# Optimization experiments

Measured on AMD Instinct MI355X. Metric: run time of the kernel, lower is better.

The kernel has to match this reference:

```python
import jax, jax.numpy as jnp
import numpy as np

NH = 12        # main attention heads (head_dim = 64)
SNH = 4        # scorer self-attention heads
ALPHA = 0.1    # static survival-score weight
EPS = 1e-8


def _linear(x, w, b):
    # torch nn.Linear: y = x @ W^T + b
    return x @ w.T + b


def _mha(x, in_w, in_b, out_w, out_b, n_heads, maskf):
    # torch nn.MultiheadAttention (batch_first, eval mode)
    B, S, D = x.shape
    hd = D // n_heads
    qkv = _linear(x, in_w, in_b)                      # [B,S,3D]
    q, k, v = jnp.split(qkv, 3, axis=-1)
    sp = lambda t: t.reshape(B, S, n_heads, hd).transpose(0, 2, 1, 3)
    q, k, v = sp(q), sp(k), sp(v)                     # [B,h,S,hd]
    scores = jnp.einsum('bhqd,bhkd->bhqk', q, k) / jnp.asarray(np.sqrt(hd), x.dtype)
    scores = jnp.where(maskf[:, None, None, :] > 0, scores, jnp.asarray(-1e9, x.dtype))
    aw = jax.nn.softmax(scores, axis=-1)
    o = jnp.einsum('bhqk,bhkd->bhqd', aw, v).transpose(0, 2, 1, 3).reshape(B, S, D)
    return _linear(o, out_w, out_b)


def _survival_scores(x, maskf, sp_w, sp_b, sa_in_w, sa_in_b, sa_out_w, sa_out_b,
                     nw1, nb1, nw2, nb2, mw1, mb1, mw2, mb2, dw1, db1, dw2, db2):
    h = _linear(x, sp_w, sp_b)                        # [B,S,256]
    h = _mha(h, sa_in_w, sa_in_b, sa_out_w, sa_out_b, SNH, maskf)
    n = jax.nn.softplus(_linear(jax.nn.relu(_linear(h, nw1, nb1)), nw2, nb2))[..., 0]
    mu = jax.nn.sigmoid(_linear(jax.nn.relu(_linear(h, mw1, mb1)), mw2, mb2))[..., 0]
    delta = jax.nn.relu(_linear(jax.nn.relu(_linear(h, dw1, db1)), dw2, db2))[..., 0]
    # S = log(N) + log(mu / mu_c) - delta, with mu_c = 1.0
    return jnp.log(n + EPS) + jnp.log(mu + EPS) - delta


def setup_inputs() -> dict:
    key = jax.random.key(0)
    ks = iter(jax.random.split(key, 40))
    W = lambda shape: jax.random.normal(next(ks), shape, jnp.float32) * 0.05
    Z = lambda shape: jnp.zeros(shape, jnp.float32)
    B, S, H, I = 2, 2048, 768, 256
    inp = {
        'x': jax.random.normal(next(ks), (B, S, H), jnp.float32),
        'mask': jnp.ones((B, S), jnp.int32),
        'qw': W((H, H)), 'qb': Z((H,)),
        'kw': W((H, H)), 'kb': Z((H,)),
        'vw': W((H, H)), 'vb': Z((H,)),
        'ow': W((H, H)), 'ob': Z((H,)),
        'sp_w': W((I, H)), 'sp_b': Z((I,)),
        'sa_in_w': W((3 * I, I)), 'sa_in_b': Z((3 * I,)),
        'sa_out_w': W((I, I)), 'sa_out_b': Z((I,)),
        'nw1': W((I // 2, I)), 'nb1': Z((I // 2,)), 'nw2': W((1, I // 2)), 'nb2': Z((1,)),
        'mw1': W((I // 2, I)), 'mb1': Z((I // 2,)), 'mw2': W((1, I // 2)), 'mb2': Z((1,)),
        'dw1': W((I // 2, I)), 'db1': Z((I // 2,)), 'dw2': W((1, I // 2)), 'db2': Z((1,)),
    }
    return inp


def reference(x, mask, qw, qb, kw, kb, vw, vb, ow, ob,
              sp_w, sp_b, sa_in_w, sa_in_b, sa_out_w, sa_out_b,
              nw1, nb1, nw2, nb2, mw1, mb1, mw2, mb2, dw1, db1, dw2, db2):
    B, S, H = x.shape
    hd = H // NH
    maskf = mask.astype(x.dtype)
    # Q/K/V projections -> [B,h,S,hd]
    sp = lambda t: t.reshape(B, S, NH, hd).transpose(0, 2, 1, 3)
    q = sp(_linear(x, qw, qb))
    k = sp(_linear(x, kw, kb))
    v = sp(_linear(x, vw, vb))
    scores = jnp.einsum('bhqd,bhkd->bhqk', q, k) / jnp.asarray(np.sqrt(hd), x.dtype)
    # survival-score bias (broadcast over heads and query positions)
    surv = _survival_scores(x, maskf, sp_w, sp_b, sa_in_w, sa_in_b, sa_out_w, sa_out_b,
                            nw1, nb1, nw2, nb2, mw1, mb1, mw2, mb2, dw1, db1, dw2, db2)
    scores = scores + ALPHA * surv[:, None, None, :]
    scores = scores + (1.0 - maskf)[:, None, None, :] * -1e9
    aw = jax.nn.softmax(scores, axis=-1)
    out = jnp.einsum('bhqk,bhkd->bhqd', aw, v).transpose(0, 2, 1, 3).reshape(B, S, H)
    return _linear(out, ow, ob)
```

## Files before the change

### kernel.cpp

```cpp
#include <hip/hip_runtime.h>
#include <math.h>

typedef __bf16 bf16;
typedef __bf16 bfrag __attribute__((ext_vector_type(8)));
typedef __bf16 bf4 __attribute__((ext_vector_type(4)));
typedef float f4 __attribute__((ext_vector_type(4)));
typedef float f16v __attribute__((ext_vector_type(16)));
typedef unsigned uint2v __attribute__((ext_vector_type(2)));

#define LOG2E 1.4426950408889634f

#define DEV static __device__ __forceinline__

DEV f4 MFMA(bfrag a, bfrag b, f4 c) {
  return __builtin_amdgcn_mfma_f32_16x16x32_bf16(a, b, c, 0, 0, 0);
}
DEV f16v MFMA32(bfrag a, bfrag b, f16v c) {
  return __builtin_amdgcn_mfma_f32_32x32x16_bf16(a, b, c, 0, 0, 0);
}
DEV float ex2(float x) { return __builtin_amdgcn_exp2f(x); }
DEV uint2v pl32(unsigned a, unsigned b) {
  return __builtin_amdgcn_permlane32_swap(a, b, false, false);
}
DEV void gload_lds16(const bf16* g, bf16* l) {
  __builtin_amdgcn_global_load_lds(
      (const __attribute__((address_space(1))) void*)g,
      (__attribute__((address_space(3))) void*)l, 16, 0, 0);
}
DEV void gload_lds4(const float* g, float* l) {
  __builtin_amdgcn_global_load_lds(
      (const __attribute__((address_space(1))) void*)g,
      (__attribute__((address_space(3))) void*)l, 4, 0, 0);
}

__global__ __launch_bounds__(256) void pack_all(
    const float* __restrict__ x, const float* __restrict__ qw, const float* __restrict__ kw,
    const float* __restrict__ vw, const float* __restrict__ ow, const float* __restrict__ sp_w,
    const float* __restrict__ sa_in_w, const float* __restrict__ sa_out_w,
    const float* __restrict__ nw1, const float* __restrict__ mw1, const float* __restrict__ dw1,
    const float* __restrict__ sp_b, const float* __restrict__ qb, const float* __restrict__ kb,
    const float* __restrict__ vb,
    const float* __restrict__ nb1, const float* __restrict__ mb1, const float* __restrict__ db1,
    const int* __restrict__ mask,
    bf16* __restrict__ xb, bf16* __restrict__ wfused, bf16* __restrict__ wob,
    bf16* __restrict__ sainb, bf16* __restrict__ saoutb,
    bf16* __restrict__ w1pack, float* __restrict__ bfused, float* __restrict__ b1pack,
    float* __restrict__ maskBias) {
  int bid = blockIdx.x;
  int tid = threadIdx.x;
  const float* src = nullptr;
  bf16* dst = nullptr;
  int rel = 0;
  if (bid < 3072)      { src = x;       dst = xb;                   rel = bid; }
  else if (bid < 3264) { src = sp_w;    dst = wfused;               rel = bid - 3072; }
  else if (bid < 3840) { src = qw;      dst = wfused + 196608;      rel = bid - 3264; }
  else if (bid < 4416) { src = kw;      dst = wfused + 786432;      rel = bid - 3840; }
  else if (bid < 4992) { src = vw;      dst = wfused + 1376256;     rel = bid - 4416; }
  else if (bid < 5568) { src = ow;      dst = wob;                  rel = bid - 4992; }
  else if (bid < 5760) { src = sa_in_w; dst = sainb;                rel = bid - 5568; }
  else if (bid < 5824) { src = sa_out_w;dst = saoutb;               rel = bid - 5760; }
  else if (bid < 5856) { src = nw1;     dst = w1pack;               rel = bid - 5824; }
  else if (bid < 5888) { src = mw1;     dst = w1pack + 32768;       rel = bid - 5856; }
  else if (bid < 5920) { src = dw1;     dst = w1pack + 2 * 32768;   rel = bid - 5888; }
  else if (bid == 5920) {
    for (int t = tid; t < 640; t += 256) {
      const float* s;
      int j;
      if (t < 64)       { s = sp_b; j = t; }
      else if (t < 256) { s = qb;   j = t - 64; }
      else if (t < 448) { s = kb;   j = t - 256; }
      else              { s = vb;   j = t - 448; }
      reinterpret_cast<float4*>(bfused)[t] = reinterpret_cast<const float4*>(s)[j];
    }
    return;
  } else if (bid == 5921) {
    if (tid < 96) {
      int which = tid / 32, j = tid % 32;
      const float* s = which == 0 ? nb1 : (which == 1 ? mb1 : db1);
      reinterpret_cast<float4*>(b1pack)[tid] = reinterpret_cast<const float4*>(s)[j];
    }
    return;
  } else {
    int idx = (bid - 5922) * 256 + tid;
    int4 m = reinterpret_cast<const int4*>(mask)[idx];
    float4 o;
    o.x = m.x > 0 ? 0.f : -1e9f * LOG2E;
    o.y = m.y > 0 ? 0.f : -1e9f * LOG2E;
    o.z = m.z > 0 ? 0.f : -1e9f * LOG2E;
    o.w = m.w > 0 ? 0.f : -1e9f * LOG2E;
    reinterpret_cast<float4*>(maskBias)[idx] = o;
    return;
  }
  int i = rel * 256 + tid;
  float4 v = reinterpret_cast<const float4*>(src)[i];
  bf4 o;
  o[0] = (bf16)v.x; o[1] = (bf16)v.y; o[2] = (bf16)v.z; o[3] = (bf16)v.w;
  reinterpret_cast<bf4*>(dst)[i] = o;
}

template<int OUTF32, int RELU>
__global__ __launch_bounds__(256) void gemm_nt(
    const bf16* __restrict__ A, int lda,
    const bf16* __restrict__ W, int ldw,
    const float* __restrict__ bias,
    void* __restrict__ C, int ldc,
    int N64, int K) {
  int lane = threadIdx.x & 63;
  int w = threadIdx.x >> 6;
  int lrow = lane & 15, lgrp = lane >> 4;
  int tn = blockIdx.x % N64, tm = blockIdx.x / N64;
  int m0 = tm * 64 + (w >> 1) * 32;
  int n0 = tn * 64 + (w & 1) * 32;
  const bf16* Ab = A + (size_t)m0 * lda + lgrp * 8;
  const bf16* Wb = W + (size_t)n0 * ldw + lgrp * 8;
  f4 acc[2][2] = {};
  for (int k0 = 0; k0 < K; k0 += 32) {
    bfrag a0 = *(const bfrag*)(Ab + (size_t)lrow * lda + k0);
    bfrag a1 = *(const bfrag*)(Ab + (size_t)(lrow + 16) * lda + k0);
    bfrag b0 = *(const bfrag*)(Wb + (size_t)lrow * ldw + k0);
    bfrag b1 = *(const bfrag*)(Wb + (size_t)(lrow + 16) * ldw + k0);
    acc[0][0] = MFMA(a0, b0, acc[0][0]);
    acc[0][1] = MFMA(a0, b1, acc[0][1]);
    acc[1][0] = MFMA(a1, b0, acc[1][0]);
    acc[1][1] = MFMA(a1, b1, acc[1][1]);
  }
#pragma unroll
  for (int mi = 0; mi < 2; mi++)
#pragma unroll
    for (int nj = 0; nj < 2; nj++) {
      int col = n0 + nj * 16 + lrow;
      float bv = bias[col];
      int rowb = m0 + mi * 16 + lgrp * 4;
#pragma unroll
      for (int i = 0; i < 4; i++) {
        float v = acc[mi][nj][i] + bv;
        if (RELU) v = fmaxf(v, 0.f);
        if (OUTF32)
          ((float*)C)[(size_t)(rowb + i) * ldc + col] = v;
        else
          ((bf16*)C)[(size_t)(rowb + i) * ldc + col] = (bf16)v;
      }
    }
}

template<int OUTF32>
__global__ __launch_bounds__(256, 2) void gemm_big(
    const bf16* __restrict__ A,
    const bf16* __restrict__ W,
    const float* __restrict__ bias,
    void* __restrict__ C, int ldc,
    int N128, int K) {
  __shared__ char smem[65536];
  int lane = threadIdx.x & 63;
  int w = threadIdx.x >> 6;
  int lrow = lane & 15, lgrp = lane >> 4;
  int tn = blockIdx.x % N128, tm = blockIdx.x / N128;
  int m0 = tm * 128, n0 = tn * 128;

  int srow = lane >> 3;
  int sslot = (lane & 7) ^ srow;

  auto stage = [&](int bufb, int k0) {
#pragma unroll
    for (int j = 0; j < 4; j++) {
      int rb = (w * 4 + j) * 8 + srow;
      gload_lds16(A + (size_t)(m0 + rb) * K + k0 + sslot * 8,
                  (bf16*)(smem + bufb + (w * 4 + j) * 1024));
      gload_lds16(W + (size_t)(n0 + rb) * K + k0 + sslot * 8,
                  (bf16*)(smem + bufb + 16384 + (w * 4 + j) * 1024));
    }
  };

  f4 acc[4][4] = {};
  int swz = (lrow & 7) << 4;
  int mbase = (w >> 1) * 64, nbase = (w & 1) * 64;

  stage(0, 0);
  __syncthreads();
  int buf = 0;
  int nt = K / 64;
  for (int t = 0; t < nt; t++) {
    int nbuf = buf ^ 32768;
    if (t + 1 < nt) stage(nbuf, (t + 1) * 64);
    const char* As = smem + buf;
    const char* Ws = smem + buf + 16384;
#pragma unroll
    for (int kb = 0; kb < 128; kb += 64) {
      bfrag a[4], b[4];
#pragma unroll
      for (int i = 0; i < 4; i++) {
        a[i] = *(const bfrag*)(As + (mbase + i * 16 + lrow) * 128 + ((kb + lgrp * 16) ^ swz));
        b[i] = *(const bfrag*)(Ws + (nbase + i * 16 + lrow) * 128 + ((kb + lgrp * 16) ^ swz));
      }
#pragma unroll
      for (int mi = 0; mi < 4; mi++)
#pragma unroll
        for (int nj = 0; nj < 4; nj++)
          acc[mi][nj] = MFMA(a[mi], b[nj], acc[mi][nj]);
    }
    __syncthreads();
    buf = nbuf;
  }

#pragma unroll
  for (int mi = 0; mi < 4; mi++)
#pragma unroll
    for (int nj = 0; nj < 4; nj++) {
      int col = n0 + nbase + nj * 16 + lrow;
      float bv = bias[col];
      int rowb = m0 + mbase + mi * 16 + lgrp * 4;
#pragma unroll
      for (int i = 0; i < 4; i++) {
        float v = acc[mi][nj][i] + bv;
        if (OUTF32)
          ((float*)C)[(size_t)(rowb + i) * ldc + col] = v;
        else
          ((bf16*)C)[(size_t)(rowb + i) * ldc + col] = (bf16)v;
      }
    }
}

__global__ __launch_bounds__(256) void vtrans(const bf16* __restrict__ V, int rs, int coff,
                                              bf16* __restrict__ Vt, int H, int S) {
  int nst = S / 64;
  int st = blockIdx.x % nst;
  int h = (blockIdx.x / nst) % H;
  int b = blockIdx.x / (nst * H);
  __shared__ bf16 tile[64][72];
  int t = threadIdx.x;
  int r = t >> 2, c = t & 3;
  const bf16* src = V + ((size_t)b * S + st * 64 + r) * rs + coff + h * 64 + c * 16;
  bfrag v0 = *(const bfrag*)(src);
  bfrag v1 = *(const bfrag*)(src + 8);
  *(bfrag*)&tile[r][c * 16] = v0;
  *(bfrag*)&tile[r][c * 16 + 8] = v1;
  __syncthreads();
  bf16* dst = Vt + (((size_t)b * H + h) * 64 + r) * S + st * 64 + c * 16;
  bfrag o0, o1;
#pragma unroll
  for (int j = 0; j < 8; j++) {
    o0[j] = tile[c * 16 + j][r];
    o1[j] = tile[c * 16 + 8 + j][r];
  }
  *(bfrag*)dst = o0;
  *(bfrag*)(dst + 8) = o1;
}

template<int SPLIT, int PARTIAL>
__global__ __launch_bounds__(256) void flash12_k(
    const bf16* __restrict__ Q, const bf16* __restrict__ Kp, int rs,
    const bf16* __restrict__ Vt, const float* __restrict__ bias,
    bf16* __restrict__ O, int ors,
    bf16* __restrict__ Opart, float* __restrict__ Lpart,
    int H, int S, float scale, int Bc) {
  int nqt = S / 128;
  int nwg8 = (gridDim.x >> 3);
  int bid0 = blockIdx.x;
  int bid = (bid0 & 7) * nwg8 + (bid0 >> 3);
  int qt = bid % nqt;
  int hh = (bid / nqt) % H;
  int b = (bid / (nqt * H)) % Bc;
  int sp = bid / (nqt * H * Bc);
  int lane = threadIdx.x & 63, w = threadIdx.x >> 6;
  int l31 = lane & 31, hf = lane >> 5;
  int q0 = qt * 128 + w * 32;
  const int kchunk = S / SPLIT;
  int k_beg = sp * kchunk;
  int swzl = (l31 & 7) << 4;

  const bf16* Qb = Q + ((size_t)b * S + q0 + l31) * rs + hh * 64 + hf * 8;
  bfrag qf[4];
#pragma unroll
  for (int c = 0; c < 4; c++) qf[c] = *(const bfrag*)(Qb + 16 * c);

  const bf16* gK0 = Kp + ((size_t)b * S + k_beg) * rs + hh * 64;
  const bf16* gV0 = Vt + (((size_t)b * H + hh) * 64) * (size_t)S + k_beg;
  const float* biasb = bias + (size_t)b * S + k_beg;

  __shared__ bf16 KT[3][4096];
  __shared__ bf16 VT[3][4096];
  __shared__ float BL[3][64];

  f16v acc0, acc1;
#pragma unroll
  for (int r = 0; r < 16; r++) { acc0[r] = 0.f; acc1[r] = 0.f; }
  float lrun = 0.f;

  int srow = lane >> 3;
  int sel = ((lane & 7) ^ srow) * 8;
  int r0 = (w * 2) * 8 + srow;
  int r1 = (w * 2 + 1) * 8 + srow;

  auto stage = [&](int bb, int trel) {
    const bf16* gK = gK0 + (size_t)trel * 64 * rs;
    const bf16* gV = gV0 + trel * 64;
    gload_lds16(gK + (size_t)r0 * rs + sel, KT[bb] + (w * 2) * 512);
    gload_lds16(gK + (size_t)r1 * rs + sel, KT[bb] + (w * 2 + 1) * 512);
    gload_lds16(gV + (size_t)r0 * S + sel, VT[bb] + (w * 2) * 512);
    gload_lds16(gV + (size_t)r1 * S + sel, VT[bb] + (w * 2 + 1) * 512);
    gload_lds4(biasb + trel * 64 + lane, BL[bb]);
  };

  const int nt = kchunk / 64;
  stage(0, 0);
  if (nt > 1) stage(1, 1);

  int buf = 0;
  for (int t = 0; t < nt; t++) {
    if (t + 1 < nt) asm volatile("s_waitcnt vmcnt(5)" ::: "memory");
    else            asm volatile("s_waitcnt vmcnt(0)" ::: "memory");
    __builtin_amdgcn_s_barrier();
    __builtin_amdgcn_sched_barrier(0);
    if (t + 2 < nt) stage(buf == 0 ? 2 : buf - 1, t + 2);

    const char* KTb = (const char*)KT[buf];
    const char* VTb = (const char*)VT[buf];
    const float* BLb = BL[buf];

    f4 blo[4], bhi[4];
#pragma unroll
    for (int g = 0; g < 4; g++) {
      blo[g] = *(const f4*)(BLb + g * 8 + hf * 4);
      bhi[g] = *(const f4*)(BLb + 32 + g * 8 + hf * 4);
    }

    f16v s_lo, s_hi;
#pragma unroll
    for (int r = 0; r < 16; r++) { s_lo[r] = 0.f; s_hi[r] = 0.f; }
    __builtin_amdgcn_s_setprio(1);
#pragma unroll
    for (int c = 0; c < 4; c++) {
      int colb = 32 * c + 16 * hf;
      bfrag klo = *(const bfrag*)(KTb + l31 * 128 + (colb ^ swzl));
      bfrag khi = *(const bfrag*)(KTb + (32 + l31) * 128 + (colb ^ swzl));
      s_lo = MFMA32(klo, qf[c], s_lo);
      s_hi = MFMA32(khi, qf[c], s_hi);
    }
    __builtin_amdgcn_s_setprio(0);

#pragma unroll
    for (int r = 0; r < 16; r++) {
      s_lo[r] = ex2(s_lo[r] * scale + blo[r >> 2][r & 3]);
      s_hi[r] = ex2(s_hi[r] * scale + bhi[r >> 2][r & 3]);
    }
    float rsum = s_lo[0] + s_hi[0];
#pragma unroll
    for (int r = 1; r < 16; r++) rsum += s_lo[r] + s_hi[r];
    rsum += __shfl_xor(rsum, 32);
    lrun += rsum;

    bfrag pb[4];
#pragma unroll
    for (int cc = 0; cc < 4; cc++) {
      const f16v& sv = (cc < 2) ? s_lo : s_hi;
      int rb = (cc & 1) * 8;
      unsigned lo0, lo1, hi0, hi1;
      asm("v_cvt_pk_bf16_f32 %0, %1, %2" : "=v"(lo0) : "v"(sv[rb + 0]), "v"(sv[rb + 1]));
      asm("v_cvt_pk_bf16_f32 %0, %1, %2" : "=v"(lo1) : "v"(sv[rb + 2]), "v"(sv[rb + 3]));
      asm("v_cvt_pk_bf16_f32 %0, %1, %2" : "=v"(hi0) : "v"(sv[rb + 4]), "v"(sv[rb + 5]));
      asm("v_cvt_pk_bf16_f32 %0, %1, %2" : "=v"(hi1) : "v"(sv[rb + 6]), "v"(sv[rb + 7]));
      uint2v e0 = pl32(lo0, hi0);
      uint2v e1 = pl32(lo1, hi1);
      union { bfrag v; unsigned u[4]; } pu;
      pu.u[0] = e0[0]; pu.u[1] = e1[0]; pu.u[2] = e0[1]; pu.u[3] = e1[1];
      pb[cc] = pu.v;
    }

    __builtin_amdgcn_s_setprio(1);
#pragma unroll
    for (int c = 0; c < 4; c++) {
      int colb = 32 * c + 16 * hf;
      bfrag v0 = *(const bfrag*)(VTb + l31 * 128 + (colb ^ swzl));
      bfrag v1 = *(const bfrag*)(VTb + (32 + l31) * 128 + (colb ^ swzl));
      acc0 = MFMA32(v0, pb[c], acc0);
      acc1 = MFMA32(v1, pb[c], acc1);
    }
    __builtin_amdgcn_s_setprio(0);

    buf = (buf == 2) ? 0 : buf + 1;
  }

  int q = q0 + l31;
  if (PARTIAL) {
    bf16* op = Opart + ((((size_t)sp * Bc + b) * H + hh) * S + q) * 64 + hf * 4;
#pragma unroll
    for (int g = 0; g < 4; g++) {
      bf4 v0, v1;
#pragma unroll
      for (int i = 0; i < 4; i++) {
        v0[i] = (bf16)acc0[4 * g + i];
        v1[i] = (bf16)acc1[4 * g + i];
      }
      *(bf4*)(op + g * 8) = v0;
      *(bf4*)(op + 32 + g * 8) = v1;
    }
    if (hf == 0)
      Lpart[(((size_t)sp * Bc + b) * H + hh) * S + q] = lrun;
  } else {
    float inv = 1.f / lrun;
    bf16* Ob = O + ((size_t)b * S + q) * ors + hh * 64 + hf * 4;
#pragma unroll
    for (int g = 0; g < 4; g++) {
      bf4 o0, o1;
#pragma unroll
      for (int i = 0; i < 4; i++) {
        o0[i] = (bf16)(acc0[4 * g + i] * inv);
        o1[i] = (bf16)(acc1[4 * g + i] * inv);
      }
      *(bf4*)(Ob + g * 8) = o0;
      *(bf4*)(Ob + 32 + g * 8) = o1;
    }
  }
}

__global__ __launch_bounds__(256) void flash_comb(
    const bf16* __restrict__ Opart, const float* __restrict__ L,
    bf16* __restrict__ O, int ors, int Hh, int S, int Bc, int nsplit) {
  int idx = blockIdx.x * 256 + threadIdx.x;
  int d4 = idx & 15;
  int q = (idx >> 4) % S;
  int hh = ((idx >> 4) / S) % Hh;
  int b = (idx >> 4) / (S * Hh);
  size_t rowstride = (size_t)Bc * Hh * S;
  size_t rbase = ((size_t)b * Hh + hh) * S + q;
  float lsum = 0.f;
  f4 o = {0.f, 0.f, 0.f, 0.f};
  for (int sp = 0; sp < nsplit; sp++) {
    lsum += L[sp * rowstride + rbase];
    bf4 a = *(const bf4*)(Opart + (sp * rowstride + rbase) * 64 + d4 * 4);
#pragma unroll
    for (int i = 0; i < 4; i++) o[i] += (float)a[i];
  }
  float inv = 1.f / lsum;
  bf4 obv;
#pragma unroll
  for (int i = 0; i < 4; i++) obv[i] = (bf16)(o[i] * inv);
  *(bf4*)(O + ((size_t)b * S + q) * ors + hh * 64 + d4 * 4) = obv;
}

__global__ __launch_bounds__(256) void surv_k(
    const bf16* __restrict__ hid,
    const float* __restrict__ nw2, const float* __restrict__ nb2,
    const float* __restrict__ mw2, const float* __restrict__ mb2,
    const float* __restrict__ dw2, const float* __restrict__ db2,
    const float* __restrict__ maskBias, float* __restrict__ biasMain) {
  int w = threadIdx.x >> 6, lane = threadIdx.x & 63;
  int row = blockIdx.x * 4 + w;
  const bf16* hr = hid + (size_t)row * 384;
  const float* W2[3] = {nw2, mw2, dw2};
  float outs[3];
#pragma unroll
  for (int t = 0; t < 3; t++) {
    float acc = (float)hr[t * 128 + lane] * W2[t][lane] +
                (float)hr[t * 128 + 64 + lane] * W2[t][64 + lane];
    for (int msk = 1; msk < 64; msk <<= 1) acc += __shfl_xor(acc, msk);
    outs[t] = acc;
  }
  if (lane == 0) {
    float xn = outs[0] + nb2[0];
    float n = (xn > 20.f) ? xn : log1pf(__expf(xn));
    float mu = 1.f / (1.f + __expf(-(outs[1] + mb2[0])));
    float delta = fmaxf(outs[2] + db2[0], 0.f);
    float surv = logf(n + 1e-8f) + logf(mu + 1e-8f) - delta;
    biasMain[row] = 0.1f * LOG2E * surv + maskBias[row];
  }
}

extern "C" void kernel_launch(void* const* d_in, const int* in_sizes, int n_in,
                              void* d_out, int out_size, void* d_ws, size_t ws_size,
                              hipStream_t stream) {
  const int B = 2, S = 2048, H = 768, I = 256;
  const int NH = 12, SNH = 4;
  const int M = B * S;
  const int NF = 2560;
  const float SC = 0.125f * LOG2E;

  const float* x = (const float*)d_in[0];
  const int* mask = (const int*)d_in[1];
  const float* qw = (const float*)d_in[2];
  const float* qb = (const float*)d_in[3];
  const float* kw = (const float*)d_in[4];
  const float* kb = (const float*)d_in[5];
  const float* vw = (const float*)d_in[6];
  const float* vb = (const float*)d_in[7];
  const float* ow = (const float*)d_in[8];
  const float* ob = (const float*)d_in[9];
  const float* sp_w = (const float*)d_in[10];
  const float* sp_b = (const float*)d_in[11];
  const float* sa_in_w = (const float*)d_in[12];
  const float* sa_in_b = (const float*)d_in[13];
  const float* sa_out_w = (const float*)d_in[14];
  const float* sa_out_b = (const float*)d_in[15];
  const float* nw1 = (const float*)d_in[16];
  const float* nb1 = (const float*)d_in[17];
  const float* nw2 = (const float*)d_in[18];
  const float* nb2 = (const float*)d_in[19];
  const float* mw1 = (const float*)d_in[20];
  const float* mb1 = (const float*)d_in[21];
  const float* mw2 = (const float*)d_in[22];
  const float* mb2 = (const float*)d_in[23];
  const float* dw1 = (const float*)d_in[24];
  const float* db1 = (const float*)d_in[25];
  const float* dw2 = (const float*)d_in[26];
  const float* db2 = (const float*)d_in[27];

  char* ws = (char*)d_ws;
  size_t off = 0;
  auto alloc = [&](size_t bytes) -> void* {
    void* p = ws + off;
    off += (bytes + 255) & ~(size_t)255;
    return p;
  };

  bf16* xb = (bf16*)alloc((size_t)M * H * 2);
  bf16* wfused = (bf16*)alloc((size_t)NF * H * 2);
  float* bfused = (float*)alloc((size_t)NF * 4);
  bf16* wob = (bf16*)alloc((size_t)H * H * 2);
  bf16* sainb = (bf16*)alloc((size_t)(3 * I) * I * 2);
  bf16* saoutb = (bf16*)alloc((size_t)I * I * 2);
  bf16* w1pack = (bf16*)alloc((size_t)384 * 256 * 2);
  float* b1pack = (float*)alloc((size_t)384 * 4);
  float* maskBias = (float*)alloc((size_t)M * 4);
  float* biasMain = (float*)alloc((size_t)M * 4);
  bf16* Cfused = (bf16*)alloc((size_t)M * NF * 2);

  const int SPM = 2, SPS = 4;
  size_t offMark = off;
  bf16* qkv_s = (bf16*)alloc((size_t)M * (3 * I) * 2);
  bf16* vt_s = (bf16*)alloc((size_t)B * SNH * 64 * S * 2);
  bf16* attn_s = (bf16*)alloc((size_t)M * I * 2);
  bf16* h1 = (bf16*)alloc((size_t)M * I * 2);
  bf16* hid = (bf16*)alloc((size_t)M * 384 * 2);
  bf16* Opart_s = (bf16*)alloc((size_t)SPS * B * SNH * S * 64 * 2);
  float* L_s = (float*)alloc((size_t)SPS * B * SNH * S * 4);
  size_t endA = off;
  off = offMark;
  bf16* vt_m = (bf16*)alloc((size_t)B * NH * 64 * S * 2);
  bf16* attn_m = (bf16*)alloc((size_t)M * H * 2);
  bf16* Opart_m = (bf16*)alloc((size_t)SPM * B * NH * S * 64 * 2);
  float* L_m = (float*)alloc((size_t)SPM * B * NH * S * 4);
  size_t endB = off;
  size_t need = endA > endB ? endA : endB;
  bool split_ok = ws_size >= need;
  (void)in_sizes; (void)n_in; (void)out_size;

  pack_all<<<5926, 256, 0, stream>>>(x, qw, kw, vw, ow, sp_w, sa_in_w, sa_out_w, nw1, mw1, dw1,
                                     sp_b, qb, kb, vb, nb1, mb1, db1, mask,
                                     xb, wfused, wob, sainb, saoutb, w1pack, bfused, b1pack,
                                     maskBias);

  gemm_big<0><<<(M / 128) * (NF / 128), 256, 0, stream>>>(xb, wfused, bfused, Cfused, NF,
                                                          NF / 128, H);

  gemm_nt<0, 0><<<(M / 64) * ((3 * I) / 64), 256, 0, stream>>>(Cfused, NF, sainb, I, sa_in_b,
                                                               qkv_s, 3 * I, (3 * I) / 64, I);
  vtrans<<<B * SNH * (S / 64), 256, 0, stream>>>(qkv_s, 3 * I, 2 * I, vt_s, SNH, S);
  if (split_ok) {
    flash12_k<SPS, 1><<<SPS * B * SNH * (S / 128), 256, 0, stream>>>(
        qkv_s, qkv_s + I, 3 * I, vt_s, maskBias, nullptr, 0, Opart_s, L_s, SNH, S, SC, B);
    flash_comb<<<(B * SNH * S * 16) / 256, 256, 0, stream>>>(Opart_s, L_s, attn_s, I, SNH, S,
                                                             B, SPS);
  } else {
    flash12_k<1, 0><<<B * SNH * (S / 128), 256, 0, stream>>>(
        qkv_s, qkv_s + I, 3 * I, vt_s, maskBias, attn_s, I, nullptr, nullptr, SNH, S, SC, B);
  }
  gemm_nt<0, 0><<<(M / 64) * (I / 64), 256, 0, stream>>>(attn_s, I, saoutb, I, sa_out_b, h1, I,
                                                         I / 64, I);
  gemm_nt<0, 1><<<(M / 64) * (384 / 64), 256, 0, stream>>>(h1, I, w1pack, I, b1pack, hid, 384,
                                                           384 / 64, I);
  surv_k<<<M / 4, 256, 0, stream>>>(hid, nw2, nb2, mw2, mb2, dw2, db2, maskBias, biasMain);

  vtrans<<<B * NH * (S / 64), 256, 0, stream>>>(Cfused, NF, 1792, vt_m, NH, S);
  if (split_ok) {
    flash12_k<SPM, 1><<<SPM * B * NH * (S / 128), 256, 0, stream>>>(
        Cfused + 256, Cfused + 1024, NF, vt_m, biasMain, nullptr, 0, Opart_m, L_m, NH, S, SC,
        B);
    flash_comb<<<(B * NH * S * 16) / 256, 256, 0, stream>>>(Opart_m, L_m, attn_m, H, NH, S, B,
                                                            SPM);
  } else {
    flash12_k<1, 0><<<B * NH * (S / 128), 256, 0, stream>>>(
        Cfused + 256, Cfused + 1024, NF, vt_m, biasMain, attn_m, H, nullptr, nullptr, NH, S,
        SC, B);
  }
  gemm_big<1><<<(M / 128) * (H / 128), 256, 0, stream>>>(attn_m, wob, ob, d_out, H,
                                                         H / 128, H);
}
```

Before: 171.4 us.

## Software-pipeline flash attention: overlap next tile's QK MFMA with previous softmax/PV

Restructures the flash attention loop so that the QK^T MFMAs for tile t are issued before the exp/convert/PV work of tile t-1. This lets matrix-core work overlap with the VALU softmax work. V and bias buffers grow from 3 to 4 stages because they must stay live one iteration longer. The cost is extra LDS and a second live score accumulator (more VGPRs), which may reduce occupancy.

```diff
diff --git a/kernel.cpp b/kernel.cpp
--- a/kernel.cpp
+++ b/kernel.cpp
@@ -247,7 +247,7 @@
 }
 
 template<int SPLIT, int PARTIAL>
-__global__ __launch_bounds__(256) void flash12_k(
+__global__ __launch_bounds__(256) void flash13_k(
     const bf16* __restrict__ Q, const bf16* __restrict__ Kp, int rs,
     const bf16* __restrict__ Vt, const float* __restrict__ bias,
     bf16* __restrict__ O, int ors,
@@ -278,8 +278,8 @@
   const float* biasb = bias + (size_t)b * S + k_beg;
 
   __shared__ bf16 KT[3][4096];
-  __shared__ bf16 VT[3][4096];
-  __shared__ float BL[3][64];
+  __shared__ bf16 VT[4][4096];
+  __shared__ float BL[4][64];
 
   f16v acc0, acc1;
 #pragma unroll
@@ -291,53 +291,28 @@
   int r0 = (w * 2) * 8 + srow;
   int r1 = (w * 2 + 1) * 8 + srow;
 
-  auto stage = [&](int bb, int trel) {
+  auto stage = [&](int kb, int vb2, int trel) {
     const bf16* gK = gK0 + (size_t)trel * 64 * rs;
     const bf16* gV = gV0 + trel * 64;
-    gload_lds16(gK + (size_t)r0 * rs + sel, KT[bb] + (w * 2) * 512);
-    gload_lds16(gK + (size_t)r1 * rs + sel, KT[bb] + (w * 2 + 1) * 512);
-    gload_lds16(gV + (size_t)r0 * S + sel, VT[bb] + (w * 2) * 512);
-    gload_lds16(gV + (size_t)r1 * S + sel, VT[bb] + (w * 2 + 1) * 512);
-    gload_lds4(biasb + trel * 64 + lane, BL[bb]);
+    gload_lds16(gK + (size_t)r0 * rs + sel, KT[kb] + (w * 2) * 512);
+    gload_lds16(gK + (size_t)r1 * rs + sel, KT[kb] + (w * 2 + 1) * 512);
+    gload_lds16(gV + (size_t)r0 * S + sel, VT[vb2] + (w * 2) * 512);
+    gload_lds16(gV + (size_t)r1 * S + sel, VT[vb2] + (w * 2 + 1) * 512);
+    gload_lds4(biasb + trel * 64 + lane, BL[vb2]);
   };
 
-  const int nt = kchunk / 64;
-  stage(0, 0);
-  if (nt > 1) stage(1, 1);
-
-  int buf = 0;
-  for (int t = 0; t < nt; t++) {
-    if (t + 1 < nt) asm volatile("s_waitcnt vmcnt(5)" ::: "memory");
-    else            asm volatile("s_waitcnt vmcnt(0)" ::: "memory");
-    __builtin_amdgcn_s_barrier();
-    __builtin_amdgcn_sched_barrier(0);
-    if (t + 2 < nt) stage(buf == 0 ? 2 : buf - 1, t + 2);
-
-    const char* KTb = (const char*)KT[buf];
-    const char* VTb = (const char*)VT[buf];
-    const float* BLb = BL[buf];
-
+  f16v s_lo, s_hi;
+#pragma unroll
+  for (int r = 0; r < 16; r++) { s_lo[r] = 0.f; s_hi[r] = 0.f; }
+
+  auto finish = [&](int pv) {
+    const float* BLb = BL[pv];
     f4 blo[4], bhi[4];
 #pragma unroll
     for (int g = 0; g < 4; g++) {
       blo[g] = *(const f4*)(BLb + g * 8 + hf * 4);
       bhi[g] = *(const f4*)(BLb + 32 + g * 8 + hf * 4);
     }
-
-    f16v s_lo, s_hi;
-#pragma unroll
-    for (int r = 0; r < 16; r++) { s_lo[r] = 0.f; s_hi[r] = 0.f; }
-    __builtin_amdgcn_s_setprio(1);
-#pragma unroll
-    for (int c = 0; c < 4; c++) {
-      int colb = 32 * c + 16 * hf;
-      bfrag klo = *(const bfrag*)(KTb + l31 * 128 + (colb ^ swzl));
-      bfrag khi = *(const bfrag*)(KTb + (32 + l31) * 128 + (colb ^ swzl));
-      s_lo = MFMA32(klo, qf[c], s_lo);
-      s_hi = MFMA32(khi, qf[c], s_hi);
-    }
-    __builtin_amdgcn_s_setprio(0);
-
 #pragma unroll
     for (int r = 0; r < 16; r++) {
       s_lo[r] = ex2(s_lo[r] * scale + blo[r >> 2][r & 3]);
@@ -366,6 +341,7 @@
       pb[cc] = pu.v;
     }
 
+    const char* VTb = (const char*)VT[pv];
     __builtin_amdgcn_s_setprio(1);
 #pragma unroll
     for (int c = 0; c < 4; c++) {
@@ -376,9 +352,46 @@
       acc1 = MFMA32(v1, pb[c], acc1);
     }
     __builtin_amdgcn_s_setprio(0);
-
-    buf = (buf == 2) ? 0 : buf + 1;
-  }
+  };
+
+  const int nt = kchunk / 64;
+  stage(0, 0, 0);
+  if (nt > 1) stage(1, 1, 1);
+
+  int kcur = 0, vcur = 0, kst = 2, vst = 2, vprev = 0;
+  for (int t = 0; t < nt; t++) {
+    if (t + 1 < nt) asm volatile("s_waitcnt vmcnt(5)" ::: "memory");
+    else            asm volatile("s_waitcnt vmcnt(0)" ::: "memory");
+    __builtin_amdgcn_s_barrier();
+    __builtin_amdgcn_sched_barrier(0);
+    if (t + 2 < nt) stage(kst, vst, t + 2);
+
+    const char* KTb = (const char*)KT[kcur];
+    f16v n_lo, n_hi;
+#pragma unroll
+    for (int r = 0; r < 16; r++) { n_lo[r] = 0.f; n_hi[r] = 0.f; }
+    __builtin_amdgcn_s_setprio(1);
+#pragma unroll
+    for (int c = 0; c < 4; c++) {
+      int colb = 32 * c + 16 * hf;
+      bfrag klo = *(const bfrag*)(KTb + l31 * 128 + (colb ^ swzl));
+      bfrag khi = *(const bfrag*)(KTb + (32 + l31) * 128 + (colb ^ swzl));
+      n_lo = MFMA32(klo, qf[c], n_lo);
+      n_hi = MFMA32(khi, qf[c], n_hi);
+    }
+    __builtin_amdgcn_s_setprio(0);
+
+    if (t > 0) finish(vprev);
+
+    s_lo = n_lo;
+    s_hi = n_hi;
+    vprev = vcur;
+    kcur = (kcur == 2) ? 0 : kcur + 1;
+    vcur = (vcur + 1) & 3;
+    kst = (kst == 2) ? 0 : kst + 1;
+    vst = (vst + 1) & 3;
+  }
+  finish(vprev);
 
   int q = q0 + l31;
   if (PARTIAL) {
@@ -556,12 +569,12 @@
                                                                qkv_s, 3 * I, (3 * I) / 64, I);
   vtrans<<<B * SNH * (S / 64), 256, 0, stream>>>(qkv_s, 3 * I, 2 * I, vt_s, SNH, S);
   if (split_ok) {
-    flash12_k<SPS, 1><<<SPS * B * SNH * (S / 128), 256, 0, stream>>>(
+    flash13_k<SPS, 1><<<SPS * B * SNH * (S / 128), 256, 0, stream>>>(
         qkv_s, qkv_s + I, 3 * I, vt_s, maskBias, nullptr, 0, Opart_s, L_s, SNH, S, SC, B);
     flash_comb<<<(B * SNH * S * 16) / 256, 256, 0, stream>>>(Opart_s, L_s, attn_s, I, SNH, S,
                                                              B, SPS);
   } else {
-    flash12_k<1, 0><<<B * SNH * (S / 128), 256, 0, stream>>>(
+    flash13_k<1, 0><<<B * SNH * (S / 128), 256, 0, stream>>>(
         qkv_s, qkv_s + I, 3 * I, vt_s, maskBias, attn_s, I, nullptr, nullptr, SNH, S, SC, B);
   }
   gemm_nt<0, 0><<<(M / 64) * (I / 64), 256, 0, stream>>>(attn_s, I, saoutb, I, sa_out_b, h1, I,
@@ -572,13 +585,13 @@
 
   vtrans<<<B * NH * (S / 64), 256, 0, stream>>>(Cfused, NF, 1792, vt_m, NH, S);
   if (split_ok) {
-    flash12_k<SPM, 1><<<SPM * B * NH * (S / 128), 256, 0, stream>>>(
+    flash13_k<SPM, 1><<<SPM * B * NH * (S / 128), 256, 0, stream>>>(
         Cfused + 256, Cfused + 1024, NF, vt_m, biasMain, nullptr, 0, Opart_m, L_m, NH, S, SC,
         B);
     flash_comb<<<(B * NH * S * 16) / 256, 256, 0, stream>>>(Opart_m, L_m, attn_m, H, NH, S, B,
                                                             SPM);
   } else {
-    flash12_k<1, 0><<<B * NH * (S / 128), 256, 0, stream>>>(
+    flash13_k<1, 0><<<B * NH * (S / 128), 256, 0, stream>>>(
         Cfused + 256, Cfused + 1024, NF, vt_m, biasMain, attn_m, H, nullptr, nullptr, NH, S,
         SC, B);
   }
```

New measurement: 175.0 us. 1.02x slower.
